# Kernel tuning notes

Hardware: AMD Instinct MI355X
Metric: run time of the kernel (lower is better)

## Reference

```python
import math
import jax, jax.numpy as jnp
import numpy as np

SEQ_LEN = 512
NUM_HEADS = 16
HEAD_DIM = 64  # hidden_size // num_heads
MAX_REL = 127


def _relative_positions_embeddings(length, depth, max_relative_position=MAX_REL):
    """Sinusoidal table gathered by clipped relative distance -> [L, L, depth]."""
    vocab = 2 * max_relative_position + 1
    pos = np.arange(vocab, dtype=np.float64)[:, None]
    i = np.arange(depth // 2, dtype=np.float64)[None, :]
    angle = pos / np.power(10000.0, 2.0 * i / depth)
    table = np.zeros((vocab, depth), dtype=np.float64)
    table[:, 0::2] = np.sin(angle)
    table[:, 1::2] = np.cos(angle)
    r = np.arange(length)
    dist = np.clip(r[None, :] - r[:, None], -max_relative_position, max_relative_position)
    final = dist + max_relative_position  # [L, L] indices into vocab
    return jnp.asarray(table[final], dtype=jnp.float32)  # [L, L, depth]

_REL_EMB = _relative_positions_embeddings(SEQ_LEN, HEAD_DIM)


def setup_inputs() -> dict:
    key = jax.random.key(0)
    ks = jax.random.split(key, 4)
    B, S, H = 8, SEQ_LEN, NUM_HEADS * HEAD_DIM
    scale = 1.0 / math.sqrt(H)
    return {
        "hidden_states": jax.random.normal(ks[0], (B, S, H), dtype=jnp.float32),
        "attention_mask": jnp.zeros((B, 1, 1, S), dtype=jnp.float32),
        "Wq": jax.random.normal(ks[1], (H, H), dtype=jnp.float32) * scale,
        "bq": jnp.zeros((H,), dtype=jnp.float32),
        "Wk": jax.random.normal(ks[2], (H, H), dtype=jnp.float32) * scale,
        "bk": jnp.zeros((H,), dtype=jnp.float32),
        "Wv": jax.random.normal(ks[3], (H, H), dtype=jnp.float32) * scale,
        "bv": jnp.zeros((H,), dtype=jnp.float32),
    }


def reference(hidden_states, attention_mask, Wq, bq, Wk, bk, Wv, bv):
    B, S, _ = hidden_states.shape
    H, D = NUM_HEADS, HEAD_DIM

    def split_heads(x):  # [B,S,H*D] -> [B,H,S,D]
        return x.reshape(B, S, H, D).transpose(0, 2, 1, 3)

    q = split_heads(hidden_states @ Wq.T + bq)
    k = split_heads(hidden_states @ Wk.T + bk)
    v = split_heads(hidden_states @ Wv.T + bv)

    rel = _REL_EMB[:S, :S, :]  # [S, S, D]

    scores = jnp.einsum("bhqd,bhkd->bhqk", q, k)
    scores = scores + jnp.einsum("bhqd,qkd->bhqk", q, rel)
    scores = scores / math.sqrt(D) + attention_mask

    probs = jax.nn.softmax(scores, axis=-1)  # dropout prob = 0.0 (eval)

    ctx = jnp.einsum("bhqk,bhkd->bhqd", probs, v)
    ctx = ctx + jnp.einsum("bhqk,qkd->bhqd", probs, rel)

    context_layer = ctx.transpose(0, 2, 1, 3).reshape(B, S, H * D)
    return context_layer, scores
```

## Files before the change

kernel.cpp:

```cpp
#include <hip/hip_runtime.h>
#include <hip/hip_bf16.h>

typedef __attribute__((ext_vector_type(4))) float f32x4;
typedef __attribute__((ext_vector_type(8))) short bf16x8;

#define NB 8
#define NS 512
#define NH 16
#define ND 64
#define HID 1024
#define NBH (NB*NH)
#define NROWS (NB*NS)

static __device__ __forceinline__ ushort f2bf(float x){
    union{float f; unsigned u;} a; a.f = x;
    unsigned r = a.u + 0x7fffu + ((a.u >> 16) & 1u);
    return (ushort)(r >> 16);
}
static __device__ __forceinline__ float bf2f(ushort x){
    union{unsigned u; float f;} a; a.u = ((unsigned)x) << 16;
    return a.f;
}

__global__ void build_tables(ushort* __restrict__ tab, ushort* __restrict__ tabT){
    int t = blockIdx.x * blockDim.x + threadIdx.x;
    if (t >= 256 * 64) return;
    int p = t >> 6, d = t & 63;
    float val = 0.f;
    if (p < 255){
        int i = d >> 1;
        float angle = (float)p / powf(10000.f, (float)i / 32.f);
        val = (d & 1) ? cosf(angle) : sinf(angle);
    }
    ushort b = f2bf(val);
    tab[p * 64 + d]  = b;
    tabT[d * 256 + p] = b;
}

__global__ void cvt_bf16(const float* __restrict__ src, ushort* __restrict__ dst, int n4){
    int i = blockIdx.x * blockDim.x + threadIdx.x;
    if (i >= n4) return;
    float4 v = reinterpret_cast<const float4*>(src)[i];
    ushort4 o;
    o.x = f2bf(v.x); o.y = f2bf(v.y); o.z = f2bf(v.z); o.w = f2bf(v.w);
    reinterpret_cast<ushort4*>(dst)[i] = o;
}

__global__ void cvt_bf16_w3(const float* __restrict__ w0, const float* __restrict__ w1,
                            const float* __restrict__ w2, ushort* __restrict__ o0,
                            ushort* __restrict__ o1, ushort* __restrict__ o2, int n4){
    int i = blockIdx.x * blockDim.x + threadIdx.x;
    if (i >= n4) return;
    const float* src = blockIdx.y == 0 ? w0 : (blockIdx.y == 1 ? w1 : w2);
    ushort* dst      = blockIdx.y == 0 ? o0 : (blockIdx.y == 1 ? o1 : o2);
    float4 v = reinterpret_cast<const float4*>(src)[i];
    ushort4 o;
    o.x = f2bf(v.x); o.y = f2bf(v.y); o.z = f2bf(v.z); o.w = f2bf(v.w);
    reinterpret_cast<ushort4*>(dst)[i] = o;
}

__global__ __launch_bounds__(256) void proj_gemm_qkv(
    const ushort* __restrict__ X,
    const ushort* __restrict__ Wqp, const ushort* __restrict__ Wkp, const ushort* __restrict__ Wvp,
    const float* __restrict__ bqp, const float* __restrict__ bkp, const float* __restrict__ bvp,
    ushort* __restrict__ outQ, ushort* __restrict__ outK, ushort* __restrict__ outV)
{
    __shared__ ushort lA[128][72];
    __shared__ ushort lB[128][72];
    int sel = blockIdx.x >> 3;
    const ushort* W   = sel == 0 ? Wqp : (sel == 1 ? Wkp : Wvp);
    const float* bias = sel == 0 ? bqp : (sel == 1 ? bkp : bvp);
    ushort* out       = sel == 0 ? outQ : (sel == 1 ? outK : outV);
    int n0 = (blockIdx.x & 7) * 128;
    int m0 = blockIdx.y * 128;
    int tid = threadIdx.x;
    int wave = tid >> 6, lane = tid & 63;
    int wr = (wave >> 1) * 64, wc = (wave & 1) * 64;
    int lrow = lane & 15, lk8 = (lane >> 4) * 8;

    f32x4 acc[4][4] = {};

    for (int k0 = 0; k0 < HID; k0 += 64){
        __syncthreads();
        #pragma unroll
        for (int i = 0; i < 4; ++i){
            int chunk = i * 256 + tid;
            int row = chunk >> 3, col = (chunk & 7) * 8;
            *reinterpret_cast<uint4*>(&lA[row][col]) =
                *reinterpret_cast<const uint4*>(&X[(size_t)(m0 + row) * HID + k0 + col]);
            *reinterpret_cast<uint4*>(&lB[row][col]) =
                *reinterpret_cast<const uint4*>(&W[(size_t)(n0 + row) * HID + k0 + col]);
        }
        __syncthreads();
        #pragma unroll
        for (int ks = 0; ks < 2; ++ks){
            bf16x8 af[4], bfr[4];
            #pragma unroll
            for (int m = 0; m < 4; ++m)
                af[m] = *reinterpret_cast<const bf16x8*>(&lA[wr + m*16 + lrow][ks*32 + lk8]);
            #pragma unroll
            for (int n = 0; n < 4; ++n)
                bfr[n] = *reinterpret_cast<const bf16x8*>(&lB[wc + n*16 + lrow][ks*32 + lk8]);
            #pragma unroll
            for (int m = 0; m < 4; ++m)
                #pragma unroll
                for (int n = 0; n < 4; ++n)
                    acc[m][n] = __builtin_amdgcn_mfma_f32_16x16x32_bf16(af[m], bfr[n], acc[m][n], 0, 0, 0);
        }
    }

    #pragma unroll
    for (int m = 0; m < 4; ++m){
        #pragma unroll
        for (int n = 0; n < 4; ++n){
            int col = n0 + wc + n*16 + lrow;
            float bv = bias[col];
            int h = col >> 6, d = col & 63;
            #pragma unroll
            for (int r = 0; r < 4; ++r){
                int mg = m0 + wr + m*16 + (lane >> 4)*4 + r;
                int b = mg >> 9, s = mg & 511;
                float val = acc[m][n][r] + bv;
                if (sel != 2)
                    out[(((size_t)(b*NH + h))*NS + s)*ND + d] = f2bf(val);
                else
                    out[(((size_t)(b*NH + h))*ND + d)*NS + s] = f2bf(val);
            }
        }
    }
}

__global__ __launch_bounds__(256) void fused_attn(
    const ushort* __restrict__ Qb, const ushort* __restrict__ Kb,
    const ushort* __restrict__ vT, const ushort* __restrict__ tab,
    const ushort* __restrict__ tabT, const float* __restrict__ mask,
    float* __restrict__ scores, float* __restrict__ ctx)
{
    __shared__ ushort pL[16][512];
    __shared__ ushort qq[16][256];
    __shared__ float  rsum[16][4];
    __shared__ float  rleft[16][4];
    __shared__ float  rright[16][4];
    ushort* pLf = &pL[0][0];
    ushort* qqf = &qq[0][0];
#define SWZ(row, col) ((col) ^ (((row)&7)<<3))

    const int bh = blockIdx.x;
    const int b = bh >> 4, h = bh & 15;
    const int q0 = blockIdx.y * 16;
    const int wave = threadIdx.x >> 6, lane = threadIdx.x & 63;
    const int lrow = lane & 15, g = lane >> 4, lk8 = g * 8;

    const ushort* Qh = Qb + (size_t)bh * NS * ND;
    const ushort* Kh = Kb + (size_t)bh * NS * ND;
    const int d = wave*16 + lrow;
    const ushort* vTh = vT + ((size_t)bh*ND + d)*NS;

    bf16x8 qf[2];
    #pragma unroll
    for (int ks = 0; ks < 2; ++ks)
        qf[ks] = *reinterpret_cast<const bf16x8*>(&Qh[(size_t)(q0 + lrow)*ND + ks*32 + lk8]);

    f32x4 acc[12];
    #pragma unroll
    for (int n = 0; n < 12; ++n) acc[n] = (f32x4){0.f, 0.f, 0.f, 0.f};

    #pragma unroll
    for (int n = 0; n < 12; ++n){
        const ushort* src = (n < 8) ? &Kh[(size_t)(wave*128 + n*16 + lrow)*ND]
                                    : &tab[(size_t)(wave*64 + (n-8)*16 + lrow)*ND];
        #pragma unroll
        for (int ks = 0; ks < 2; ++ks){
            bf16x8 kf = *reinterpret_cast<const bf16x8*>(&src[ks*32 + lk8]);
            acc[n] = __builtin_amdgcn_mfma_f32_16x16x32_bf16(kf, qf[ks], acc[n], 0, 0, 0);
        }
    }

    bf16x8 vpre[8];
    #pragma unroll
    for (int i = 0; i < 8; ++i)
        vpre[i] = *reinterpret_cast<const bf16x8*>(&vTh[i*64 + lk8]);

    #pragma unroll
    for (int n = 8; n < 12; ++n){
        ushort4 w;
        w.x = f2bf(acc[n][0]); w.y = f2bf(acc[n][1]);
        w.z = f2bf(acc[n][2]); w.w = f2bf(acc[n][3]);
        int col = wave*64 + (n-8)*16 + g*4;
        *reinterpret_cast<ushort4*>(&qqf[lrow*256 + SWZ(lrow, col)]) = w;
    }
    __syncthreads();

    const int q = q0 + lrow;
    float st = 0.f, sl = 0.f, sr = 0.f;
    #pragma unroll
    for (int n = 0; n < 8; ++n){
        int kbase = wave*128 + n*16 + g*4;
        float4 mk4 = *reinterpret_cast<const float4*>(&mask[b*NS + kbase]);
        float mk[4] = {mk4.x, mk4.y, mk4.z, mk4.w};
        f32x4 sv;
        #pragma unroll
        for (int r = 0; r < 4; ++r){
            int k = kbase + r;
            int dd = min(127, max(-127, k - q));
            float val = (acc[n][r] + bf2f(qqf[lrow*256 + SWZ(lrow, dd + 127)])) * 0.125f + mk[r];
            sv[r] = val;
            float e = __expf(val);
            acc[n][r] = e;
            st += e;
            if (k <= q - 127) sl += e;
            if (k >= q + 127) sr += e;
        }
        __builtin_nontemporal_store(sv,
            reinterpret_cast<f32x4*>(&scores[((size_t)bh*NS + q)*NS + kbase]));
    }
    st += __shfl_xor(st, 16); st += __shfl_xor(st, 32);
    sl += __shfl_xor(sl, 16); sl += __shfl_xor(sl, 32);
    sr += __shfl_xor(sr, 16); sr += __shfl_xor(sr, 32);
    if (lane < 16){
        rsum[lrow][wave] = st;
        rleft[lrow][wave] = sl;
        rright[lrow][wave] = sr;
    }
    __syncthreads();

    float T  = rsum[lrow][0] + rsum[lrow][1] + rsum[lrow][2] + rsum[lrow][3];
    float iv = 1.f / T;
    float Lv = (rleft[lrow][0] + rleft[lrow][1] + rleft[lrow][2] + rleft[lrow][3]) * iv;
    float Rv = (rright[lrow][0] + rright[lrow][1] + rright[lrow][2] + rright[lrow][3]) * iv;

    #pragma unroll
    for (int n = 0; n < 8; ++n){
        int kbase = wave*128 + n*16 + g*4;
        ushort4 w;
        w.x = f2bf(acc[n][0] * iv); w.y = f2bf(acc[n][1] * iv);
        w.z = f2bf(acc[n][2] * iv); w.w = f2bf(acc[n][3] * iv);
        *reinterpret_cast<ushort4*>(&pLf[lrow*512 + SWZ(lrow, kbase)]) = w;
    }
    if (wave == 0 && lane < 16){
        qqf[lrow*256 + SWZ(lrow, 0)]   = f2bf(Lv);
        qqf[lrow*256 + SWZ(lrow, 254)] = f2bf(Rv);
    }
    __syncthreads();

    for (int idx = threadIdx.x; idx < 16*256; idx += 256){
        int row = idx >> 8, j = idx & 255;
        if (j == 0 || j >= 254) continue;
        int col = q0 + row + j - 127;
        qqf[row*256 + SWZ(row, j)] =
            (col >= 0 && col < NS) ? pLf[row*512 + SWZ(row, col)] : (ushort)0;
    }
    __syncthreads();

    const ushort* tTd = tabT + (size_t)d*256;
    f32x4 o0 = (f32x4){0.f,0.f,0.f,0.f};
    f32x4 o1 = (f32x4){0.f,0.f,0.f,0.f};
    #pragma unroll
    for (int i = 0; i < 8; ++i){
        int k0 = i*64;
        bf16x8 pa0 = *reinterpret_cast<const bf16x8*>(&pLf[lrow*512 + SWZ(lrow, k0 + lk8)]);
        o0 = __builtin_amdgcn_mfma_f32_16x16x32_bf16(pa0, vpre[i], o0, 0, 0, 0);
        bf16x8 bv1 = *reinterpret_cast<const bf16x8*>(&vTh[k0 + 32 + lk8]);
        bf16x8 pa1 = *reinterpret_cast<const bf16x8*>(&pLf[lrow*512 + SWZ(lrow, k0 + 32 + lk8)]);
        o1 = __builtin_amdgcn_mfma_f32_16x16x32_bf16(pa1, bv1, o1, 0, 0, 0);
    }
    #pragma unroll
    for (int k0 = 0; k0 < 256; k0 += 64){
        bf16x8 bv0 = *reinterpret_cast<const bf16x8*>(&tTd[k0 + lk8]);
        bf16x8 pa0 = *reinterpret_cast<const bf16x8*>(&qqf[lrow*256 + SWZ(lrow, k0 + lk8)]);
        o0 = __builtin_amdgcn_mfma_f32_16x16x32_bf16(pa0, bv0, o0, 0, 0, 0);
        bf16x8 bv1 = *reinterpret_cast<const bf16x8*>(&tTd[k0 + 32 + lk8]);
        bf16x8 pa1 = *reinterpret_cast<const bf16x8*>(&qqf[lrow*256 + SWZ(lrow, k0 + 32 + lk8)]);
        o1 = __builtin_amdgcn_mfma_f32_16x16x32_bf16(pa1, bv1, o1, 0, 0, 0);
    }
    #pragma unroll
    for (int r = 0; r < 4; ++r){
        int qo = q0 + g*4 + r;
        __builtin_nontemporal_store(o0[r] + o1[r],
            &ctx[((size_t)b*NS + qo)*HID + h*ND + d]);
    }
#undef SWZ
}

extern "C" void kernel_launch(void* const* d_in, const int* in_sizes, int n_in,
                              void* d_out, int out_size, void* d_ws, size_t ws_size,
                              hipStream_t stream)
{
    const float* x    = (const float*)d_in[0];
    const float* mask = (const float*)d_in[1];
    const float* Wq   = (const float*)d_in[2];
    const float* bq   = (const float*)d_in[3];
    const float* Wk   = (const float*)d_in[4];
    const float* bk   = (const float*)d_in[5];
    const float* Wv   = (const float*)d_in[6];
    const float* bv   = (const float*)d_in[7];

    float* out = (float*)d_out;
    float* ctx    = out;
    float* scores = out + (size_t)NB*NS*HID;

    char* ws = (char*)d_ws;
    ushort* x_bf  = (ushort*)ws;  ws += (size_t)NROWS*HID*2;
    ushort* wq_bf = (ushort*)ws;  ws += (size_t)HID*HID*2;
    ushort* wk_bf = (ushort*)ws;  ws += (size_t)HID*HID*2;
    ushort* wv_bf = (ushort*)ws;  ws += (size_t)HID*HID*2;
    ushort* q_bf  = (ushort*)ws;  ws += (size_t)NBH*NS*ND*2;
    ushort* k_bf  = (ushort*)ws;  ws += (size_t)NBH*NS*ND*2;
    ushort* vT_bf = (ushort*)ws;  ws += (size_t)NBH*NS*ND*2;
    ushort* tab   = (ushort*)ws;  ws += 256*64*2;
    ushort* tabT  = (ushort*)ws;  ws += 64*256*2;

    build_tables<<<64, 256, 0, stream>>>(tab, tabT);

    cvt_bf16<<<(NROWS*HID/4 + 255)/256, 256, 0, stream>>>(x, x_bf, NROWS*HID/4);
    cvt_bf16_w3<<<dim3((HID*HID/4 + 255)/256, 3), 256, 0, stream>>>(
        Wq, Wk, Wv, wq_bf, wk_bf, wv_bf, HID*HID/4);

    proj_gemm_qkv<<<dim3(24, 32), 256, 0, stream>>>(
        x_bf, wq_bf, wk_bf, wv_bf, bq, bk, bv, q_bf, k_bf, vT_bf);

    fused_attn<<<dim3(NBH, NS/16), 256, 0, stream>>>(
        q_bf, k_bf, vT_bf, tab, tabT, mask, scores, ctx);
}
```

Measured before the change: 180.2 us.

## Use async global-to-LDS loads in QKV GEMM and reorder attention stores

The projection GEMM now stages tiles through direct global-to-LDS loads, which removes the register round trip, and drops the row padding the LDS layout needs for that. In the attention kernel the scores stores are deferred until after the softmax barriers and held in registers, V fragments are loaded inside the PV loop instead of being prefetched, wave priority is raised around the MFMA loops, and the ctx stores become ordinary stores. Removing the padding may bring back LDS bank conflicts on fragment reads, and keeping all scores in registers raises register pressure.

```diff
diff --git a/kernel.cpp b/kernel.cpp
--- a/kernel.cpp
+++ b/kernel.cpp
@@ -20,6 +20,15 @@
 static __device__ __forceinline__ float bf2f(ushort x){
     union{unsigned u; float f;} a; a.u = ((unsigned)x) << 16;
     return a.f;
+}
+
+static __device__ __forceinline__ void async_copy16(const void* gsrc, void* ldst){
+    __builtin_amdgcn_global_load_lds(
+        reinterpret_cast<const __attribute__((address_space(1))) unsigned int*>(
+            reinterpret_cast<uintptr_t>(gsrc)),
+        reinterpret_cast<__attribute__((address_space(3))) unsigned int*>(
+            reinterpret_cast<uintptr_t>(ldst)),
+        16, 0, 0);
 }
 
 __global__ void build_tables(ushort* __restrict__ tab, ushort* __restrict__ tabT){
@@ -65,8 +74,8 @@
     const float* __restrict__ bqp, const float* __restrict__ bkp, const float* __restrict__ bvp,
     ushort* __restrict__ outQ, ushort* __restrict__ outK, ushort* __restrict__ outV)
 {
-    __shared__ ushort lA[128][72];
-    __shared__ ushort lB[128][72];
+    __shared__ ushort lA[128][64];
+    __shared__ ushort lB[128][64];
     int sel = blockIdx.x >> 3;
     const ushort* W   = sel == 0 ? Wqp : (sel == 1 ? Wkp : Wvp);
     const float* bias = sel == 0 ? bqp : (sel == 1 ? bkp : bvp);
@@ -78,18 +87,19 @@
     int wr = (wave >> 1) * 64, wc = (wave & 1) * 64;
     int lrow = lane & 15, lk8 = (lane >> 4) * 8;
 
+    const int srow = tid >> 3;
+    const int scol = (tid & 7) * 8;
+    char* ldsA = (char*)(&lA[0][0]) + wave * 1024;
+    char* ldsB = (char*)(&lB[0][0]) + wave * 1024;
+
     f32x4 acc[4][4] = {};
 
     for (int k0 = 0; k0 < HID; k0 += 64){
         __syncthreads();
         #pragma unroll
-        for (int i = 0; i < 4; ++i){
-            int chunk = i * 256 + tid;
-            int row = chunk >> 3, col = (chunk & 7) * 8;
-            *reinterpret_cast<uint4*>(&lA[row][col]) =
-                *reinterpret_cast<const uint4*>(&X[(size_t)(m0 + row) * HID + k0 + col]);
-            *reinterpret_cast<uint4*>(&lB[row][col]) =
-                *reinterpret_cast<const uint4*>(&W[(size_t)(n0 + row) * HID + k0 + col]);
+        for (int p = 0; p < 4; ++p){
+            async_copy16(&X[(size_t)(m0 + srow + p*32) * HID + k0 + scol], ldsA + p*4096);
+            async_copy16(&W[(size_t)(n0 + srow + p*32) * HID + k0 + scol], ldsB + p*4096);
         }
         __syncthreads();
         #pragma unroll
@@ -155,6 +165,7 @@
     const ushort* Kh = Kb + (size_t)bh * NS * ND;
     const int d = wave*16 + lrow;
     const ushort* vTh = vT + ((size_t)bh*ND + d)*NS;
+    const int q = q0 + lrow;
 
     bf16x8 qf[2];
     #pragma unroll
@@ -175,11 +186,6 @@
             acc[n] = __builtin_amdgcn_mfma_f32_16x16x32_bf16(kf, qf[ks], acc[n], 0, 0, 0);
         }
     }
-
-    bf16x8 vpre[8];
-    #pragma unroll
-    for (int i = 0; i < 8; ++i)
-        vpre[i] = *reinterpret_cast<const bf16x8*>(&vTh[i*64 + lk8]);
 
     #pragma unroll
     for (int n = 8; n < 12; ++n){
@@ -191,28 +197,25 @@
     }
     __syncthreads();
 
-    const int q = q0 + lrow;
     float st = 0.f, sl = 0.f, sr = 0.f;
+    f32x4 sv[8];
     #pragma unroll
     for (int n = 0; n < 8; ++n){
         int kbase = wave*128 + n*16 + g*4;
         float4 mk4 = *reinterpret_cast<const float4*>(&mask[b*NS + kbase]);
         float mk[4] = {mk4.x, mk4.y, mk4.z, mk4.w};
-        f32x4 sv;
         #pragma unroll
         for (int r = 0; r < 4; ++r){
             int k = kbase + r;
             int dd = min(127, max(-127, k - q));
             float val = (acc[n][r] + bf2f(qqf[lrow*256 + SWZ(lrow, dd + 127)])) * 0.125f + mk[r];
-            sv[r] = val;
+            sv[n][r] = val;
             float e = __expf(val);
             acc[n][r] = e;
             st += e;
             if (k <= q - 127) sl += e;
             if (k >= q + 127) sr += e;
         }
-        __builtin_nontemporal_store(sv,
-            reinterpret_cast<f32x4*>(&scores[((size_t)bh*NS + q)*NS + kbase]));
     }
     st += __shfl_xor(st, 16); st += __shfl_xor(st, 32);
     sl += __shfl_xor(sl, 16); sl += __shfl_xor(sl, 32);
@@ -252,14 +255,22 @@
     }
     __syncthreads();
 
+    #pragma unroll
+    for (int n = 0; n < 8; ++n){
+        int kbase = wave*128 + n*16 + g*4;
+        __builtin_nontemporal_store(sv[n],
+            reinterpret_cast<f32x4*>(&scores[((size_t)bh*NS + q)*NS + kbase]));
+    }
+
     const ushort* tTd = tabT + (size_t)d*256;
     f32x4 o0 = (f32x4){0.f,0.f,0.f,0.f};
     f32x4 o1 = (f32x4){0.f,0.f,0.f,0.f};
-    #pragma unroll
-    for (int i = 0; i < 8; ++i){
-        int k0 = i*64;
+    __builtin_amdgcn_s_setprio(1);
+    #pragma unroll
+    for (int k0 = 0; k0 < NS; k0 += 64){
+        bf16x8 bv0 = *reinterpret_cast<const bf16x8*>(&vTh[k0 + lk8]);
         bf16x8 pa0 = *reinterpret_cast<const bf16x8*>(&pLf[lrow*512 + SWZ(lrow, k0 + lk8)]);
-        o0 = __builtin_amdgcn_mfma_f32_16x16x32_bf16(pa0, vpre[i], o0, 0, 0, 0);
+        o0 = __builtin_amdgcn_mfma_f32_16x16x32_bf16(pa0, bv0, o0, 0, 0, 0);
         bf16x8 bv1 = *reinterpret_cast<const bf16x8*>(&vTh[k0 + 32 + lk8]);
         bf16x8 pa1 = *reinterpret_cast<const bf16x8*>(&pLf[lrow*512 + SWZ(lrow, k0 + 32 + lk8)]);
         o1 = __builtin_amdgcn_mfma_f32_16x16x32_bf16(pa1, bv1, o1, 0, 0, 0);
@@ -273,11 +284,11 @@
         bf16x8 pa1 = *reinterpret_cast<const bf16x8*>(&qqf[lrow*256 + SWZ(lrow, k0 + 32 + lk8)]);
         o1 = __builtin_amdgcn_mfma_f32_16x16x32_bf16(pa1, bv1, o1, 0, 0, 0);
     }
+    __builtin_amdgcn_s_setprio(0);
     #pragma unroll
     for (int r = 0; r < 4; ++r){
         int qo = q0 + g*4 + r;
-        __builtin_nontemporal_store(o0[r] + o1[r],
-            &ctx[((size_t)b*NS + qo)*HID + h*ND + d]);
+        ctx[((size_t)b*NS + qo)*HID + h*ND + d] = o0[r] + o1[r];
     }
 #undef SWZ
 }
```

New measurement: 199.3 us. +10.6%, slower.
